# Optimization experiments

Hardware: AMD Instinct MI355X
Metric: run time of the kernel (lower is better)

The kernel has to match this reference:

```python
import jax, jax.numpy as jnp
import numpy as np

N, E = 50000, 200000
EMB_ATOM, EMB_EDGE = 256, 512
IN_SIZE = 2 * EMB_ATOM + EMB_EDGE  # 1024


def setup_inputs() -> dict:
    key = jax.random.key(0)
    k_h, k_m, k_i, k_j, k_w = jax.random.split(key, 5)
    h = jax.random.normal(k_h, (N, EMB_ATOM), dtype=jnp.float32)
    m_ij = jax.random.normal(k_m, (E, EMB_EDGE), dtype=jnp.float32)
    idx_i = jax.random.randint(k_i, (E,), 0, N, dtype=jnp.int64)
    idx_j = jax.random.randint(k_j, (E,), 0, N, dtype=jnp.int64)
    # bias-free Dense weight, stored as (in, out) for x @ W
    W = jax.random.normal(k_w, (IN_SIZE, EMB_EDGE), dtype=jnp.float32) * (1.0 / np.sqrt(IN_SIZE))
    return {"h": h, "m_ij": m_ij, "idx_i": idx_i, "idx_j": idx_j, "W": W}


def reference(h, m_ij, idx_i, idx_j, W):
    h_i = h[idx_i]                                   # (E, emb_atom)
    h_j = h[idx_j]                                   # (E, emb_atom)
    x = jnp.concatenate([h_i, h_j, m_ij], axis=-1)   # (E, 2*emb_atom + emb_edge)
    out = x @ W                                      # (E, emb_edge), bias-free Dense
    return jax.nn.silu(out)
```

## Files before the change

### kernel.cpp

```cpp
#include <hip/hip_runtime.h>
#include <hip/hip_bf16.h>
#include <math.h>

#define EMB_ATOM 256
#define EMB_EDGE 512
#define K_TOT    1024

typedef __attribute__((ext_vector_type(8))) short bf16x8;
typedef __attribute__((ext_vector_type(4))) float f32x4;
typedef struct { unsigned short x, y, z, w; } us4;

static __device__ __forceinline__ unsigned short f2bf(float f) {
  union { float f; unsigned u; } x; x.f = f;
  unsigned r = x.u + 0x7fffu + ((x.u >> 16) & 1u);
  return (unsigned short)(r >> 16);
}
static __device__ __forceinline__ float bf2f(unsigned short b) {
  union { unsigned u; float f; } x; x.u = ((unsigned)b) << 16; return x.f;
}
static __device__ __forceinline__ us4 f4bf(float4 v) {
  us4 o; o.x = f2bf(v.x); o.y = f2bf(v.y); o.z = f2bf(v.z); o.w = f2bf(v.w); return o;
}
static __device__ __forceinline__ bf16x8 cvt8(float4 a, float4 b) {
  union { bf16x8 v; __hip_bfloat162 h[4]; } u;
  u.h[0] = __float22bfloat162_rn(make_float2(a.x, a.y));
  u.h[1] = __float22bfloat162_rn(make_float2(a.z, a.w));
  u.h[2] = __float22bfloat162_rn(make_float2(b.x, b.y));
  u.h[3] = __float22bfloat162_rn(make_float2(b.z, b.w));
  return u.v;
}
static __device__ __forceinline__ void gload_lds16(const void* g, void* l) {
  __builtin_amdgcn_global_load_lds(
      (const __attribute__((address_space(1))) unsigned int*)g,
      (__attribute__((address_space(3))) unsigned int*)l, 16, 0, 0);
}
static __device__ __forceinline__ float silu_f(float x) { return x / (1.f + __expf(-x)); }

__global__ __launch_bounds__(256) void cvt_h_kernel(const float* __restrict__ h,
                                                    unsigned short* __restrict__ hb, int n4) {
  int i = blockIdx.x * 256 + threadIdx.x;
  if (i >= n4) return;
  const float4 v = ((const float4*)h)[i];
  ((us4*)hb)[i] = f4bf(v);
}

__global__ __launch_bounds__(256) void cvt_wh_kernel(const float* __restrict__ W,
                                                     unsigned short* __restrict__ Wt_h) {
  int o = blockIdx.x * 256 + threadIdx.x;
  int c = o >> 8, k = o & 255;
  float v = (c < 512) ? W[(size_t)k * EMB_EDGE + c]
                      : W[(size_t)(256 + k) * EMB_EDGE + (c - 512)];
  Wt_h[o] = f2bf(v);
}

__global__ __launch_bounds__(256) void cvt_wm_kernel(const float* __restrict__ W,
                                                     unsigned short* __restrict__ Wt_m) {
  int o = blockIdx.x * 256 + threadIdx.x;
  int c = o >> 9, k = o & 511;
  Wt_m[o] = f2bf(W[(size_t)(512 + k) * EMB_EDGE + c]);
}

__global__ __launch_bounds__(256) void hgemm_kernel(
    const unsigned short* __restrict__ hb,
    const unsigned short* __restrict__ Wt_h,
    unsigned short* __restrict__ H12, int N)
{
  __shared__ unsigned short As[2][128 * 64];
  __shared__ unsigned short Bs[2][128 * 64];
  const int bn = blockIdx.x;
  const int bm = blockIdx.y;
  const int row0 = bm * 128;
  const int tid = threadIdx.x, wave = tid >> 6, lane = tid & 63;
  const int srow = lane >> 3;
  const int schunk = ((lane & 7) ^ srow) * 8;

  size_t abase[4]; size_t bbase[4];
#pragma unroll
  for (int i = 0; i < 4; ++i) {
    int r = wave * 32 + i * 8 + srow;
    int e = row0 + r; if (e >= N) e = N - 1;
    abase[i] = (size_t)e * EMB_ATOM;
    bbase[i] = (size_t)(bn * 128 + r) * EMB_ATOM;
  }

  const int wr = wave >> 1, wc = wave & 1, fr = lane & 15, fq = lane >> 4;
  const int fs = fr & 7;

  f32x4 acc[4][4];
#pragma unroll
  for (int m = 0; m < 4; ++m)
#pragma unroll
    for (int n = 0; n < 4; ++n) acc[m][n] = (f32x4)0.f;

#pragma unroll
  for (int i = 0; i < 4; ++i) {
    gload_lds16(hb + abase[i] + schunk,   &As[0][(wave * 32 + i * 8) * 64 + lane * 8]);
    gload_lds16(Wt_h + bbase[i] + schunk, &Bs[0][(wave * 32 + i * 8) * 64 + lane * 8]);
  }
  __syncthreads();

  int cur = 0;
  for (int kt = 0; kt < 4; ++kt) {
    int nxt = cur ^ 1;
    if (kt < 3) {
      int kk = (kt + 1) * 64;
#pragma unroll
      for (int i = 0; i < 4; ++i) {
        gload_lds16(hb + abase[i] + kk + schunk,   &As[nxt][(wave * 32 + i * 8) * 64 + lane * 8]);
        gload_lds16(Wt_h + bbase[i] + kk + schunk, &Bs[nxt][(wave * 32 + i * 8) * 64 + lane * 8]);
      }
    }
#pragma unroll
    for (int ks = 0; ks < 2; ++ks) {
      bf16x8 a[4], b[4];
#pragma unroll
      for (int m = 0; m < 4; ++m)
        a[m] = *(const bf16x8*)(&As[cur][(wr * 64 + m * 16 + fr) * 64 + (((ks * 4 + fq) ^ fs) << 3)]);
#pragma unroll
      for (int n = 0; n < 4; ++n)
        b[n] = *(const bf16x8*)(&Bs[cur][(wc * 64 + n * 16 + fr) * 64 + (((ks * 4 + fq) ^ fs) << 3)]);
#pragma unroll
      for (int m = 0; m < 4; ++m)
#pragma unroll
        for (int n = 0; n < 4; ++n)
          acc[m][n] = __builtin_amdgcn_mfma_f32_16x16x32_bf16(a[m], b[n], acc[m][n], 0, 0, 0);
    }
    __syncthreads();
    cur = nxt;
  }

#pragma unroll
  for (int m = 0; m < 4; ++m) {
    int er0 = row0 + wr * 64 + m * 16 + fq * 4;
#pragma unroll
    for (int n = 0; n < 4; ++n) {
      int col = bn * 128 + wc * 64 + n * 16 + fr;
      f32x4 v = acc[m][n];
#pragma unroll
      for (int j = 0; j < 4; ++j) {
        int e = er0 + j;
        if (e < N) H12[(size_t)e * 1024 + col] = f2bf(v[j]);
      }
    }
  }
}

__global__ __launch_bounds__(256, 3) void mgemm_kernel(
    const float* __restrict__ m_ij,
    const int* __restrict__ idx_i,
    const int* __restrict__ idx_j,
    const unsigned short* __restrict__ Wt_m,
    const unsigned short* __restrict__ H12,
    float* __restrict__ out, int E, int nbm)
{
  __shared__ __align__(16) unsigned short As[128 * 64];
  __shared__ __align__(16) unsigned short Bs[2][128 * 64];

  int b  = blockIdx.x;
  int bm = (b >> 5) * 8 + (b & 7);
  int bn = (b >> 3) & 3;
  if (bm >= nbm) return;
  const int row0 = bm * 128;
  const int tid = threadIdx.x, wave = tid >> 6, lane = tid & 63;
  const int fr = lane & 15, fq = lane >> 4;
  const int wr = wave >> 1, wc = wave & 1;

  const int ar = tid >> 1;
  const int ah = tid & 1;
  int ae = row0 + ar; if (ae >= E) ae = E - 1;
  const float* aptr = m_ij + (size_t)ae * EMB_EDGE + ah * 32;
  const unsigned short* bsrc[4];
  unsigned bdst[4];
#pragma unroll
  for (int i = 0; i < 4; ++i) {
    int r = wave * 32 + i * 8 + (lane >> 3);
    int sc = (lane & 7) ^ (r & 7);
    bsrc[i] = Wt_m + (size_t)(bn * 128 + r) * 512 + sc * 8;
    bdst[i] = (wave * 32 + i * 8) * 64;
  }

  f32x4 acc[4][4];
#pragma unroll
  for (int m = 0; m < 4; ++m)
#pragma unroll
    for (int n = 0; n < 4; ++n) acc[m][n] = (f32x4)0.f;

  float4 ra[8];
#pragma unroll
  for (int i = 0; i < 4; ++i) {
    ra[2 * i]     = *(const float4*)(aptr + i * 8);
    ra[2 * i + 1] = *(const float4*)(aptr + i * 8 + 4);
  }
#pragma unroll
  for (int i = 0; i < 4; ++i) gload_lds16(bsrc[i], &Bs[0][bdst[i]]);

#pragma unroll
  for (int kt = 0; kt < 8; ++kt) {
    bf16x8 aw[4];
#pragma unroll
    for (int i = 0; i < 4; ++i) aw[i] = cvt8(ra[2 * i], ra[2 * i + 1]);
    const int kkn = (kt < 7 ? kt + 1 : 7) * 64;
#pragma unroll
    for (int i = 0; i < 4; ++i) {
      ra[2 * i]     = *(const float4*)(aptr + kkn + i * 8);
      ra[2 * i + 1] = *(const float4*)(aptr + kkn + i * 8 + 4);
    }
    __builtin_amdgcn_sched_barrier(0);
    __builtin_amdgcn_s_barrier();
    __builtin_amdgcn_sched_barrier(0);
#pragma unroll
    for (int i = 0; i < 4; ++i)
      *(bf16x8*)(&As[ar * 64 + (((ah * 4 + i) ^ (ar & 7)) << 3)]) = aw[i];
#pragma unroll
    for (int i = 0; i < 4; ++i) gload_lds16(bsrc[i] + kkn, &Bs[(kt + 1) & 1][bdst[i]]);
    __builtin_amdgcn_sched_barrier(0);
    asm volatile("s_waitcnt lgkmcnt(0)" ::: "memory");
    asm volatile("s_waitcnt vmcnt(12)" ::: "memory");
    __builtin_amdgcn_sched_barrier(0);
    __builtin_amdgcn_s_barrier();
    __builtin_amdgcn_sched_barrier(0);
#pragma unroll
    for (int ks = 0; ks < 2; ++ks) {
      bf16x8 afr[4], bfr[4];
#pragma unroll
      for (int n = 0; n < 4; ++n)
        bfr[n] = *(const bf16x8*)(&Bs[kt & 1][(wc * 64 + n * 16 + fr) * 64 + (((ks * 4 + fq) ^ (fr & 7)) << 3)]);
#pragma unroll
      for (int m = 0; m < 4; ++m)
        afr[m] = *(const bf16x8*)(&As[(wr * 64 + m * 16 + fr) * 64 + (((ks * 4 + fq) ^ (fr & 7)) << 3)]);
#pragma unroll
      for (int m = 0; m < 4; ++m)
#pragma unroll
        for (int n = 0; n < 4; ++n)
          acc[m][n] = __builtin_amdgcn_mfma_f32_16x16x32_bf16(afr[m], bfr[n], acc[m][n], 0, 0, 0);
    }
    __builtin_amdgcn_sched_barrier(0);
  }

#pragma unroll
  for (int m = 0; m < 4; ++m) {
#pragma unroll
    for (int j = 0; j < 4; ++j) {
      int e = row0 + wr * 64 + m * 16 + fq * 4 + j;
      if (e < E) {
        size_t gi = (size_t)idx_i[e] * 1024;
        size_t gj = (size_t)idx_j[e] * 1024 + 512;
#pragma unroll
        for (int n = 0; n < 4; ++n) {
          int col = bn * 128 + wc * 64 + n * 16 + fr;
          float x = acc[m][n][j] + bf2f(H12[gi + col]) + bf2f(H12[gj + col]);
          out[(size_t)e * EMB_EDGE + col] = silu_f(x);
        }
      }
    }
  }
}

__global__ __launch_bounds__(256) void cvt_wt_kernel(const float* __restrict__ W,
                                                     unsigned short* __restrict__ Wt) {
  int o = blockIdx.x * 256 + threadIdx.x;
  int n = o >> 10, k = o & 1023;
  Wt[o] = f2bf(W[(size_t)k * EMB_EDGE + n]);
}

__global__ __launch_bounds__(256) void gemm_gather_kernel(
    const unsigned short* __restrict__ hb,
    const float* __restrict__ m_ij,
    const int* __restrict__ idx_i,
    const int* __restrict__ idx_j,
    const unsigned short* __restrict__ Wt,
    float* __restrict__ out, int E)
{
  __shared__ unsigned short As[128 * 64];
  __shared__ unsigned short Bs[128 * 64];
  const int bn = blockIdx.x, bm = blockIdx.y;
  const int tid = threadIdx.x, wave = tid >> 6, lane = tid & 63;
  const int row0 = bm * 128;
  const int srow = lane >> 3, scol = (lane & 7) * 8;
  int arow[4], aii[4], ajj[4];
#pragma unroll
  for (int i = 0; i < 4; ++i) {
    int r = wave * 32 + i * 8 + srow;
    int e = row0 + r; if (e >= E) e = E - 1;
    arow[i] = r; aii[i] = idx_i[e]; ajj[i] = idx_j[e];
  }
  const int wr = wave >> 1, wc = wave & 1, fr = lane & 15, fq = lane >> 4;
  f32x4 acc[4][4];
#pragma unroll
  for (int m = 0; m < 4; ++m)
#pragma unroll
    for (int n = 0; n < 4; ++n) acc[m][n] = (f32x4)0.f;
  for (int kt = 0; kt < 16; ++kt) {
    __syncthreads();
#pragma unroll
    for (int i = 0; i < 4; ++i) {
      int nl = wave * 32 + i * 8 + srow;
      gload_lds16(Wt + (size_t)(bn * 128 + nl) * K_TOT + kt * 64 + scol, &Bs[nl * 64 + scol]);
    }
    if (kt < 8) {
      const int kh = (kt & 3) * 64;
#pragma unroll
      for (int i = 0; i < 4; ++i) {
        int idx = (kt < 4) ? aii[i] : ajj[i];
        gload_lds16(hb + (size_t)idx * EMB_ATOM + kh + scol, &As[arow[i] * 64 + scol]);
      }
    } else {
      const int kk = (kt - 8) * 64;
#pragma unroll
      for (int it = 0; it < 8; ++it) {
        int flat = it * 1024 + tid * 4;
        int r = flat >> 6, c = flat & 63;
        int e = row0 + r; if (e >= E) e = E - 1;
        const float4 v = *(const float4*)(m_ij + (size_t)e * EMB_EDGE + kk + c);
        *(us4*)(&As[r * 64 + c]) = f4bf(v);
      }
    }
    __syncthreads();
#pragma unroll
    for (int ks = 0; ks < 2; ++ks) {
      bf16x8 a[4], b[4];
#pragma unroll
      for (int m = 0; m < 4; ++m)
        a[m] = *(const bf16x8*)(&As[(wr * 64 + m * 16 + fr) * 64 + ks * 32 + fq * 8]);
#pragma unroll
      for (int n = 0; n < 4; ++n)
        b[n] = *(const bf16x8*)(&Bs[(wc * 64 + n * 16 + fr) * 64 + ks * 32 + fq * 8]);
#pragma unroll
      for (int m = 0; m < 4; ++m)
#pragma unroll
        for (int n = 0; n < 4; ++n)
          acc[m][n] = __builtin_amdgcn_mfma_f32_16x16x32_bf16(a[m], b[n], acc[m][n], 0, 0, 0);
    }
  }
#pragma unroll
  for (int m = 0; m < 4; ++m) {
    int er0 = row0 + wr * 64 + m * 16 + fq * 4;
#pragma unroll
    for (int n = 0; n < 4; ++n) {
      int col = bn * 128 + wc * 64 + n * 16 + fr;
      f32x4 v = acc[m][n];
#pragma unroll
      for (int j = 0; j < 4; ++j) {
        int e = er0 + j;
        if (e < E) out[(size_t)e * EMB_EDGE + col] = silu_f(v[j]);
      }
    }
  }
}

extern "C" void kernel_launch(void* const* d_in, const int* in_sizes, int n_in,
                              void* d_out, int out_size, void* d_ws, size_t ws_size,
                              hipStream_t stream) {
  const float* h    = (const float*)d_in[0];
  const float* m_ij = (const float*)d_in[1];
  const int*   ii   = (const int*)d_in[2];
  const int*   jj   = (const int*)d_in[3];
  const float* W    = (const float*)d_in[4];
  float* out = (float*)d_out;

  const int hsz = in_sizes[0];
  const int N   = hsz / EMB_ATOM;
  const int E   = in_sizes[2];

  unsigned short* hb   = (unsigned short*)d_ws;
  unsigned short* Wt_h = hb + hsz;
  unsigned short* Wt_m = Wt_h + 1024 * 256;
  unsigned short* H12  = Wt_m + 512 * 512;
  size_t need = ((size_t)hsz + 1024 * 256 + 512 * 512 + (size_t)N * 1024) * 2;

  if (ws_size >= need) {
    cvt_h_kernel<<<(hsz / 4 + 255) / 256, 256, 0, stream>>>(h, hb, hsz / 4);
    cvt_wh_kernel<<<1024, 256, 0, stream>>>(W, Wt_h);
    cvt_wm_kernel<<<1024, 256, 0, stream>>>(W, Wt_m);
    int nbmh = (N + 127) / 128;
    hgemm_kernel<<<dim3(8, nbmh), 256, 0, stream>>>(hb, Wt_h, H12, N);
    int nbm  = (E + 127) / 128;
    int ngrp = (nbm + 7) / 8;
    mgemm_kernel<<<ngrp * 32, 256, 0, stream>>>(m_ij, ii, jj, Wt_m, H12, out, E, nbm);
  } else {
    unsigned short* Wt  = (unsigned short*)d_ws;
    unsigned short* hbf = Wt + 512 * 1024;
    cvt_wt_kernel<<<(512 * 1024) / 256, 256, 0, stream>>>(W, Wt);
    cvt_h_kernel<<<(hsz / 4 + 255) / 256, 256, 0, stream>>>(h, hbf, hsz / 4);
    dim3 grid(4, (E + 127) / 128);
    gemm_gather_kernel<<<grid, 256, 0, stream>>>(hbf, m_ij, ii, jj, Wt, out, E);
  }
}
```

Baseline: 536.5 us.

## Load m_ij A-fragments straight to registers and use 8-wave blocks

The edge GEMM no longer stages the m_ij tile through shared memory. Each lane loads its MFMA A-fragment directly from global fp32, converts it to bf16 in registers, and double-buffers those registers across k-tiles. The block grows to 512 threads (8 waves, each covering 32 rows by 64 columns), and only the weight tile stays in LDS, with a single barrier per k-tile. This removes the LDS writes, reads and one barrier for A, at the cost of less contiguous per-lane global loads of m_ij and a smaller per-wave tile.

```diff
diff --git a/kernel.cpp b/kernel.cpp
--- a/kernel.cpp
+++ b/kernel.cpp
@@ -145,7 +145,7 @@
   }
 }
 
-__global__ __launch_bounds__(256, 3) void mgemm_kernel(
+__global__ __launch_bounds__(512, 4) void mgemm_kernel(
     const float* __restrict__ m_ij,
     const int* __restrict__ idx_i,
     const int* __restrict__ idx_j,
@@ -153,7 +153,6 @@
     const unsigned short* __restrict__ H12,
     float* __restrict__ out, int E, int nbm)
 {
-  __shared__ __align__(16) unsigned short As[128 * 64];
   __shared__ __align__(16) unsigned short Bs[2][128 * 64];
 
   int b  = blockIdx.x;
@@ -165,83 +164,104 @@
   const int fr = lane & 15, fq = lane >> 4;
   const int wr = wave >> 1, wc = wave & 1;
 
-  const int ar = tid >> 1;
-  const int ah = tid & 1;
-  int ae = row0 + ar; if (ae >= E) ae = E - 1;
-  const float* aptr = m_ij + (size_t)ae * EMB_EDGE + ah * 32;
-  const unsigned short* bsrc[4];
-  unsigned bdst[4];
-#pragma unroll
-  for (int i = 0; i < 4; ++i) {
-    int r = wave * 32 + i * 8 + (lane >> 3);
+  const unsigned short* bsrc[2];
+#pragma unroll
+  for (int i = 0; i < 2; ++i) {
+    int r = wave * 16 + i * 8 + (lane >> 3);
     int sc = (lane & 7) ^ (r & 7);
     bsrc[i] = Wt_m + (size_t)(bn * 128 + r) * 512 + sc * 8;
-    bdst[i] = (wave * 32 + i * 8) * 64;
-  }
-
-  f32x4 acc[4][4];
-#pragma unroll
-  for (int m = 0; m < 4; ++m)
+  }
+
+  const float* ap[2];
+#pragma unroll
+  for (int m = 0; m < 2; ++m) {
+    int e = row0 + wr * 32 + m * 16 + fr; if (e >= E) e = E - 1;
+    ap[m] = m_ij + (size_t)e * EMB_EDGE + fq * 8;
+  }
+
+  f32x4 acc[2][4];
+#pragma unroll
+  for (int m = 0; m < 2; ++m)
 #pragma unroll
     for (int n = 0; n < 4; ++n) acc[m][n] = (f32x4)0.f;
 
-  float4 ra[8];
-#pragma unroll
-  for (int i = 0; i < 4; ++i) {
-    ra[2 * i]     = *(const float4*)(aptr + i * 8);
-    ra[2 * i + 1] = *(const float4*)(aptr + i * 8 + 4);
-  }
-#pragma unroll
-  for (int i = 0; i < 4; ++i) gload_lds16(bsrc[i], &Bs[0][bdst[i]]);
+  float4 rg[2][2][2][2];
+
+#pragma unroll
+  for (int i = 0; i < 2; ++i)
+    gload_lds16(bsrc[i], &Bs[0][(wave * 16 + i * 8) * 64 + lane * 8]);
+  __syncthreads();
+#pragma unroll
+  for (int m = 0; m < 2; ++m)
+#pragma unroll
+    for (int ks = 0; ks < 2; ++ks) {
+      rg[0][m][ks][0] = *(const float4*)(ap[m] + ks * 32);
+      rg[0][m][ks][1] = *(const float4*)(ap[m] + ks * 32 + 4);
+    }
+  __builtin_amdgcn_sched_barrier(0);
 
 #pragma unroll
   for (int kt = 0; kt < 8; ++kt) {
-    bf16x8 aw[4];
-#pragma unroll
-    for (int i = 0; i < 4; ++i) aw[i] = cvt8(ra[2 * i], ra[2 * i + 1]);
+    const int cur = kt & 1, nxt = cur ^ 1;
     const int kkn = (kt < 7 ? kt + 1 : 7) * 64;
 #pragma unroll
-    for (int i = 0; i < 4; ++i) {
-      ra[2 * i]     = *(const float4*)(aptr + kkn + i * 8);
-      ra[2 * i + 1] = *(const float4*)(aptr + kkn + i * 8 + 4);
-    }
+    for (int i = 0; i < 2; ++i)
+      gload_lds16(bsrc[i] + kkn, &Bs[nxt][(wave * 16 + i * 8) * 64 + lane * 8]);
     __builtin_amdgcn_sched_barrier(0);
+
+    {
+      bf16x8 afr[2], bfr[4];
+#pragma unroll
+      for (int m = 0; m < 2; ++m)
+        afr[m] = cvt8(rg[cur][m][0][0], rg[cur][m][0][1]);
+#pragma unroll
+      for (int n = 0; n < 4; ++n) {
+        const int row = wc * 64 + n * 16 + fr;
+        bfr[n] = *(const bf16x8*)(&Bs[cur][row * 64 + ((fq ^ (row & 7)) << 3)]);
+      }
+#pragma unroll
+      for (int m = 0; m < 2; ++m)
+#pragma unroll
+        for (int n = 0; n < 4; ++n)
+          acc[m][n] = __builtin_amdgcn_mfma_f32_16x16x32_bf16(afr[m], bfr[n], acc[m][n], 0, 0, 0);
+    }
+#pragma unroll
+    for (int m = 0; m < 2; ++m)
+#pragma unroll
+      for (int ks = 0; ks < 2; ++ks) {
+        rg[nxt][m][ks][0] = *(const float4*)(ap[m] + kkn + ks * 32);
+        rg[nxt][m][ks][1] = *(const float4*)(ap[m] + kkn + ks * 32 + 4);
+      }
+    __builtin_amdgcn_sched_barrier(0);
+
+    {
+      bf16x8 afr[2], bfr[4];
+#pragma unroll
+      for (int m = 0; m < 2; ++m)
+        afr[m] = cvt8(rg[cur][m][1][0], rg[cur][m][1][1]);
+#pragma unroll
+      for (int n = 0; n < 4; ++n) {
+        const int row = wc * 64 + n * 16 + fr;
+        bfr[n] = *(const bf16x8*)(&Bs[cur][row * 64 + (((4 + fq) ^ (row & 7)) << 3)]);
+      }
+#pragma unroll
+      for (int m = 0; m < 2; ++m)
+#pragma unroll
+        for (int n = 0; n < 4; ++n)
+          acc[m][n] = __builtin_amdgcn_mfma_f32_16x16x32_bf16(afr[m], bfr[n], acc[m][n], 0, 0, 0);
+    }
+    __builtin_amdgcn_sched_barrier(0);
+
+    asm volatile("s_waitcnt vmcnt(8) lgkmcnt(0)" ::: "memory");
     __builtin_amdgcn_s_barrier();
     __builtin_amdgcn_sched_barrier(0);
-#pragma unroll
-    for (int i = 0; i < 4; ++i)
-      *(bf16x8*)(&As[ar * 64 + (((ah * 4 + i) ^ (ar & 7)) << 3)]) = aw[i];
-#pragma unroll
-    for (int i = 0; i < 4; ++i) gload_lds16(bsrc[i] + kkn, &Bs[(kt + 1) & 1][bdst[i]]);
-    __builtin_amdgcn_sched_barrier(0);
-    asm volatile("s_waitcnt lgkmcnt(0)" ::: "memory");
-    asm volatile("s_waitcnt vmcnt(12)" ::: "memory");
-    __builtin_amdgcn_sched_barrier(0);
-    __builtin_amdgcn_s_barrier();
-    __builtin_amdgcn_sched_barrier(0);
-#pragma unroll
-    for (int ks = 0; ks < 2; ++ks) {
-      bf16x8 afr[4], bfr[4];
-#pragma unroll
-      for (int n = 0; n < 4; ++n)
-        bfr[n] = *(const bf16x8*)(&Bs[kt & 1][(wc * 64 + n * 16 + fr) * 64 + (((ks * 4 + fq) ^ (fr & 7)) << 3)]);
-#pragma unroll
-      for (int m = 0; m < 4; ++m)
-        afr[m] = *(const bf16x8*)(&As[(wr * 64 + m * 16 + fr) * 64 + (((ks * 4 + fq) ^ (fr & 7)) << 3)]);
-#pragma unroll
-      for (int m = 0; m < 4; ++m)
-#pragma unroll
-        for (int n = 0; n < 4; ++n)
-          acc[m][n] = __builtin_amdgcn_mfma_f32_16x16x32_bf16(afr[m], bfr[n], acc[m][n], 0, 0, 0);
-    }
-    __builtin_amdgcn_sched_barrier(0);
-  }
-
-#pragma unroll
-  for (int m = 0; m < 4; ++m) {
+  }
+
+#pragma unroll
+  for (int m = 0; m < 2; ++m) {
 #pragma unroll
     for (int j = 0; j < 4; ++j) {
-      int e = row0 + wr * 64 + m * 16 + fq * 4 + j;
+      int e = row0 + wr * 32 + m * 16 + fq * 4 + j;
       if (e < E) {
         size_t gi = (size_t)idx_i[e] * 1024;
         size_t gj = (size_t)idx_j[e] * 1024 + 512;
@@ -376,7 +396,7 @@
     hgemm_kernel<<<dim3(8, nbmh), 256, 0, stream>>>(hb, Wt_h, H12, N);
     int nbm  = (E + 127) / 128;
     int ngrp = (nbm + 7) / 8;
-    mgemm_kernel<<<ngrp * 32, 256, 0, stream>>>(m_ij, ii, jj, Wt_m, H12, out, E, nbm);
+    mgemm_kernel<<<ngrp * 32, 512, 0, stream>>>(m_ij, ii, jj, Wt_m, H12, out, E, nbm);
   } else {
     unsigned short* Wt  = (unsigned short*)d_ws;
     unsigned short* hbf = Wt + 512 * 1024;
```

After: 622.5 us. 16.0% more time.
